# Performance work log

Hardware: AMD Instinct MI355X
Metric: run time of the kernel (lower is better)

## Reference

```python
import jax, jax.numpy as jnp
import numpy as np

N = 100000   # nodes
E = 1600000  # edges
D_IN, D_H, D_OUT = 128, 128, 64
BN_EPS = 1e-5


def setup_inputs() -> dict:
    key = jax.random.key(0)
    ks = jax.random.split(key, 12)

    def lin_w(k, fan_in, shape):
        s = 1.0 / np.sqrt(fan_in)
        return jax.random.uniform(k, shape, jnp.float32, -s, s)

    return {
        "x": jax.random.normal(ks[0], (N, D_IN), jnp.float32),
        "edge_index": jax.random.randint(ks[1], (2, E), 0, N, dtype=jnp.int64),
        "edge_weight": jax.random.uniform(ks[2], (E,), jnp.float32),
        "W1": lin_w(ks[3], D_IN, (D_IN, D_H)),
        "b1": jnp.zeros((D_H,), jnp.float32),
        "W2": lin_w(ks[4], D_H, (D_H, D_H)),
        "b2": jnp.zeros((D_H,), jnp.float32),
        "W3": lin_w(ks[5], D_H, (D_H, D_OUT)),
        "b3": jnp.zeros((D_OUT,), jnp.float32),
        "gamma1": jnp.ones((D_H,), jnp.float32),
        "beta1": jnp.zeros((D_H,), jnp.float32),
        "gamma2": jnp.ones((D_H,), jnp.float32),
        "beta2": jnp.zeros((D_H,), jnp.float32),
    }


def _gcn_conv(x, src, dst, w, W, b):
    # PyG GCNConv: x' = D^{-1/2} (A + I) D^{-1/2} (x W) + b, self-loop weight 1
    n = x.shape[0]
    h = x @ W                                   # [N, d_out]
    loop = jnp.arange(n, dtype=src.dtype)
    s = jnp.concatenate([src, loop])            # [E+N]
    d = jnp.concatenate([dst, loop])
    ww = jnp.concatenate([w, jnp.ones((n,), w.dtype)])
    deg = jax.ops.segment_sum(ww, d, num_segments=n)          # in-degree at targets
    dinv = jnp.where(deg > 0, jax.lax.rsqrt(deg), 0.0)
    norm = dinv[s] * ww * dinv[d]               # [E+N]
    msg = h[s] * norm[:, None]                  # gather + scale
    out = jax.ops.segment_sum(msg, d, num_segments=n)
    return out + b


def _batch_norm(x, gamma, beta):
    mean = jnp.mean(x, axis=0)
    var = jnp.mean(jnp.square(x - mean), axis=0)  # biased, as BatchNorm uses
    return (x - mean) * jax.lax.rsqrt(var + BN_EPS) * gamma + beta


def reference(x, edge_index, edge_weight, W1, b1, W2, b2, W3, b3,
              gamma1, beta1, gamma2, beta2):
    src, dst = edge_index[0], edge_index[1]
    h = _gcn_conv(x, src, dst, edge_weight, W1, b1)
    h = jax.nn.relu(_batch_norm(h, gamma1, beta1))
    h = _gcn_conv(h, src, dst, edge_weight, W2, b2)
    h = jax.nn.relu(_batch_norm(h, gamma2, beta2))
    return _gcn_conv(h, src, dst, edge_weight, W3, b3)
```

## Files before the change

### kernel.cpp

```cpp
#include <hip/hip_runtime.h>
#include <hip/hip_fp16.h>
#include <cstdint>
#include <cstddef>

#define BN_EPS 1e-5f
#define FPSCALE 268435456.0f

typedef _Float16 half8 __attribute__((ext_vector_type(8)));
typedef float floatx4 __attribute__((ext_vector_type(4)));

__device__ __forceinline__ float loadS(const __half* p) { return __half2float(*p); }
__device__ __forceinline__ float2 load2(const __half* p) {
    return __half22float2(*(const __half2*)p);
}
__device__ __forceinline__ void storeS(float* p, float v) { *p = v; }
__device__ __forceinline__ void storeS(__half* p, float v) { *p = __float2half(v); }
__device__ __forceinline__ void store2(float* p, float a, float b) {
    *(float2*)p = make_float2(a, b);
}
__device__ __forceinline__ void store2(__half* p, float a, float b) {
    *(__half2*)p = __floats2half2_rn(a, b);
}
__device__ __forceinline__ float wn_of(unsigned v) {
    __half_raw hr; hr.x = (unsigned short)(v & 0x7fffu);
    return __half2float((__half)hr);
}

static __device__ __forceinline__ int load_edge(const void* ei, int mode64, long long pos) {
    if (mode64) return (int)((const long long*)ei)[pos];
    return ((const int*)ei)[pos];
}

__global__ __launch_bounds__(256) void init_kernel(const unsigned* __restrict__ eiw, int nwords,
                                                   int* __restrict__ mode,
                                                   unsigned long long* __restrict__ packed, int N,
                                                   const float* __restrict__ W1,
                                                   const float* __restrict__ W2,
                                                   const float* __restrict__ W3,
                                                   _Float16* __restrict__ WT1,
                                                   _Float16* __restrict__ WT2,
                                                   _Float16* __restrict__ WT3, int nb) {
    __shared__ unsigned red[256];
    const int bid = (int)blockIdx.x;
    const int tid = (int)threadIdx.x;
    if (bid < nb) {
        int i = bid * 256 + tid;
        if (i < N) packed[i] = 0ULL;
        return;
    }
    if (bid == nb) {
        unsigned m = 0;
        for (int i = 1 + 2 * tid; i < nwords; i += 512) m |= eiw[i];
        red[tid] = m;
        __syncthreads();
        for (int s = 128; s > 0; s >>= 1) {
            if (tid < s) red[tid] |= red[tid + s];
            __syncthreads();
        }
        if (tid == 0) mode[0] = (red[0] == 0) ? 1 : 0;
        return;
    }
    const int t_ = bid - nb - 1;
    if (t_ < 64) {
        int t = t_ * 256 + tid;
        int n = t / 128, k = t % 128;
        WT1[t] = (_Float16)W1[k * 128 + n];
    } else if (t_ < 128) {
        int t = (t_ - 64) * 256 + tid;
        int n = t / 128, k = t % 128;
        WT2[t] = (_Float16)W2[k * 128 + n];
    } else {
        int t = (t_ - 128) * 256 + tid;
        int n = t / 128, k = t % 128;
        WT3[t] = (_Float16)W3[k * 64 + n];
    }
}

template <int M, bool BN, typename TI>
__device__ __forceinline__ void gemm_body(int gbid, const TI* __restrict__ X,
                                          const _Float16* __restrict__ WTg,
                                          const float* __restrict__ sc,
                                          const float* __restrict__ sh,
                                          __half* __restrict__ Hout, int N,
                                          _Float16* WT ) {
    constexpr int CT = M / 16;
    constexpr int LDK = 136;

    for (int t = threadIdx.x; t < M * 16; t += 256) {
        int n = t / 16, seg = t % 16;
        *(half8*)&WT[n * LDK + seg * 8] = *(const half8*)&WTg[n * 128 + seg * 8];
    }
    __syncthreads();

    const int wave = (int)threadIdx.x >> 6;
    const int lane = (int)threadIdx.x & 63;
    const int qd = lane >> 4;
    const int ln = lane & 15;
    const int tile0 = gbid * 64 + wave * 16;
    int ar = tile0 + ln;
    if (ar >= N) ar = N - 1;

    half8 aF[4];
    const TI* xr = X + (size_t)ar * 128 + qd * 8;
#pragma unroll
    for (int kb = 0; kb < 4; ++kb) {
        float vv[8];
        if constexpr (sizeof(TI) == 4) {
            float4 v0 = *(const float4*)(xr + kb * 32);
            float4 v1 = *(const float4*)(xr + kb * 32 + 4);
            vv[0] = v0.x; vv[1] = v0.y; vv[2] = v0.z; vv[3] = v0.w;
            vv[4] = v1.x; vv[5] = v1.y; vv[6] = v1.z; vv[7] = v1.w;
        } else {
            half8 raw = *(const half8*)(xr + kb * 32);
#pragma unroll
            for (int j = 0; j < 8; ++j) vv[j] = (float)raw[j];
        }
        if (BN) {
            const int kbase = kb * 32 + qd * 8;
#pragma unroll
            for (int j = 0; j < 8; ++j)
                vv[j] = fmaxf(fmaf(vv[j], sc[kbase + j], sh[kbase + j]), 0.0f);
        }
        half8 a;
#pragma unroll
        for (int j = 0; j < 8; ++j) a[j] = (_Float16)vv[j];
        aF[kb] = a;
    }

#pragma unroll
    for (int ct = 0; ct < CT; ++ct) {
        floatx4 acc = {0.0f, 0.0f, 0.0f, 0.0f};
#pragma unroll
        for (int kb = 0; kb < 4; ++kb) {
            half8 b = *(const half8*)&WT[(ct * 16 + ln) * LDK + kb * 32 + qd * 8];
            acc = __builtin_amdgcn_mfma_f32_16x16x32_f16(aF[kb], b, acc, 0, 0, 0);
        }
#pragma unroll
        for (int r = 0; r < 4; ++r) {
            int orow = tile0 + qd * 4 + r;
            if (orow < N) Hout[(size_t)orow * M + ct * 16 + ln] = __float2half(acc[r]);
        }
    }
}

__global__ __launch_bounds__(256) void hist_gemm1_kernel(const void* __restrict__ ei,
                                                         const float* __restrict__ ew,
                                                         unsigned long long* __restrict__ packed,
                                                         unsigned char* __restrict__ rank,
                                                         const int* __restrict__ mode, int E, int GB,
                                                         const float* __restrict__ X,
                                                         const _Float16* __restrict__ WT1g,
                                                         __half* __restrict__ Hout, int N) {
    __shared__ _Float16 WT[128 * 136];
    if ((int)blockIdx.x < GB) {
        gemm_body<128, false, float>(blockIdx.x, X, WT1g, nullptr, nullptr, Hout, N, WT);
        return;
    }
    int e = ((int)blockIdx.x - GB) * 256 + (int)threadIdx.x;
    if (e >= E) return;
    int md = *mode;
    int d = load_edge(ei, md, (long long)E + e);
    unsigned long long contrib = (1ULL << 40) | (unsigned long long)(ew[e] * FPSCALE);
    unsigned long long old = atomicAdd(&packed[d], contrib);
    unsigned r = (unsigned)(old >> 40);
    rank[e] = (unsigned char)(r < 63u ? r : 63u);
}

__global__ __launch_bounds__(256) void unpack_kernel(const unsigned long long* __restrict__ packed,
                                                     float* __restrict__ dinv,
                                                     int* __restrict__ cnt, int N) {
    int i = (int)blockIdx.x * 256 + (int)threadIdx.x;
    if (i < N) {
        unsigned long long p = packed[i];
        int c = (int)(p >> 40);
        cnt[i] = c < 64 ? c : 64;
        dinv[i] = rsqrtf(1.0f + (float)(p & 0xFFFFFFFFFFULL) * (1.0f / FPSCALE));
    }
}

__global__ __launch_bounds__(256) void scatter_zero_kernel(const void* __restrict__ ei,
                                                           const float* __restrict__ ew,
                                                           const float* __restrict__ dinv,
                                                           const unsigned char* __restrict__ rank,
                                                           unsigned* __restrict__ edata,
                                                           const int* __restrict__ mode, int E, int EBK,
                                                           float* __restrict__ gsum,
                                                           float* __restrict__ gsq,
                                                           int* __restrict__ tickets) {
    if ((int)blockIdx.x == EBK) {
        if (threadIdx.x < 128) { gsum[threadIdx.x] = 0.0f; gsq[threadIdx.x] = 0.0f; }
        if (threadIdx.x < 2) tickets[threadIdx.x] = 0;
        return;
    }
    int e = (int)blockIdx.x * 256 + (int)threadIdx.x;
    if (e >= E) return;
    int md = *mode;
    int s = load_edge(ei, md, e);
    int d = load_edge(ei, md, (long long)E + e);
    float wn = dinv[s] * ew[e] * dinv[d];
    unsigned hb = (unsigned)__half_as_ushort(__float2half(wn)) & 0x7fffu;
    edata[((size_t)d << 6) + rank[e]] = ((unsigned)s << 15) | hb;
}

template <int D, bool BIAS, typename TY>
__global__ __launch_bounds__(256) void agg_kernel(const __half* __restrict__ H,
                                                  const unsigned* __restrict__ edata,
                                                  const int* __restrict__ cnt,
                                                  const float* __restrict__ dinv,
                                                  const float* __restrict__ bias,
                                                  TY* __restrict__ Y, int N) {
    constexpr int VPT = D / 64;
    const int lane = (int)threadIdx.x & 63;
    const int i = (int)blockIdx.x * 4 + ((int)threadIdx.x >> 6);
    if (i >= N) return;
    const int c0 = lane * VPT;
    const float di = dinv[i];
    const float dii = di * di;

    float acc0, acc1 = 0.0f;
    if constexpr (VPT == 2) {
        float2 h = load2(H + (size_t)i * D + c0);
        acc0 = dii * h.x;
        acc1 = dii * h.y;
    } else {
        acc0 = dii * loadS(H + (size_t)i * D + c0);
    }

    const int n = cnt[i];
    unsigned ev = 0;
    if (lane < n) ev = edata[((size_t)i << 6) + lane];
    for (int j = 0; j < n; j += 8) {
        const unsigned e0 = __shfl(ev, j),     e1 = __shfl(ev, j + 1);
        const unsigned e2 = __shfl(ev, j + 2), e3 = __shfl(ev, j + 3);
        const unsigned e4 = __shfl(ev, j + 4), e5 = __shfl(ev, j + 5);
        const unsigned e6 = __shfl(ev, j + 6), e7 = __shfl(ev, j + 7);
        if constexpr (VPT == 2) {
            float2 h0 = load2(H + (size_t)(e0 >> 15) * D + c0);
            float2 h1 = load2(H + (size_t)(e1 >> 15) * D + c0);
            float2 h2 = load2(H + (size_t)(e2 >> 15) * D + c0);
            float2 h3 = load2(H + (size_t)(e3 >> 15) * D + c0);
            float2 h4 = load2(H + (size_t)(e4 >> 15) * D + c0);
            float2 h5 = load2(H + (size_t)(e5 >> 15) * D + c0);
            float2 h6 = load2(H + (size_t)(e6 >> 15) * D + c0);
            float2 h7 = load2(H + (size_t)(e7 >> 15) * D + c0);
            acc0 = fmaf(wn_of(e0), h0.x, acc0); acc1 = fmaf(wn_of(e0), h0.y, acc1);
            acc0 = fmaf(wn_of(e1), h1.x, acc0); acc1 = fmaf(wn_of(e1), h1.y, acc1);
            acc0 = fmaf(wn_of(e2), h2.x, acc0); acc1 = fmaf(wn_of(e2), h2.y, acc1);
            acc0 = fmaf(wn_of(e3), h3.x, acc0); acc1 = fmaf(wn_of(e3), h3.y, acc1);
            acc0 = fmaf(wn_of(e4), h4.x, acc0); acc1 = fmaf(wn_of(e4), h4.y, acc1);
            acc0 = fmaf(wn_of(e5), h5.x, acc0); acc1 = fmaf(wn_of(e5), h5.y, acc1);
            acc0 = fmaf(wn_of(e6), h6.x, acc0); acc1 = fmaf(wn_of(e6), h6.y, acc1);
            acc0 = fmaf(wn_of(e7), h7.x, acc0); acc1 = fmaf(wn_of(e7), h7.y, acc1);
        } else {
            float h0 = loadS(H + (size_t)(e0 >> 15) * D + c0);
            float h1 = loadS(H + (size_t)(e1 >> 15) * D + c0);
            float h2 = loadS(H + (size_t)(e2 >> 15) * D + c0);
            float h3 = loadS(H + (size_t)(e3 >> 15) * D + c0);
            float h4 = loadS(H + (size_t)(e4 >> 15) * D + c0);
            float h5 = loadS(H + (size_t)(e5 >> 15) * D + c0);
            float h6 = loadS(H + (size_t)(e6 >> 15) * D + c0);
            float h7 = loadS(H + (size_t)(e7 >> 15) * D + c0);
            acc0 = fmaf(wn_of(e0), h0, acc0);
            acc0 = fmaf(wn_of(e1), h1, acc0);
            acc0 = fmaf(wn_of(e2), h2, acc0);
            acc0 = fmaf(wn_of(e3), h3, acc0);
            acc0 = fmaf(wn_of(e4), h4, acc0);
            acc0 = fmaf(wn_of(e5), h5, acc0);
            acc0 = fmaf(wn_of(e6), h6, acc0);
            acc0 = fmaf(wn_of(e7), h7, acc0);
        }
    }

    if constexpr (VPT == 2) {
        if (BIAS) { acc0 += bias[c0]; acc1 += bias[c0 + 1]; }
        store2(Y + (size_t)i * D + c0, acc0, acc1);
    } else {
        if (BIAS) acc0 += bias[c0];
        storeS(Y + (size_t)i * D + c0, acc0);
    }
}

template <int M, bool BN, typename TI, bool ZERO>
__global__ __launch_bounds__(256) void gemm_mfma_kernel(const TI* __restrict__ X,
                                                        const _Float16* __restrict__ WTg,
                                                        const float* __restrict__ sc,
                                                        const float* __restrict__ sh,
                                                        __half* __restrict__ Hout, int N,
                                                        float* __restrict__ gsum,
                                                        float* __restrict__ gsq, int GB) {
    __shared__ _Float16 WT[M * 136];
    if (ZERO && (int)blockIdx.x == GB) {
        if (threadIdx.x < 128) { gsum[threadIdx.x] = 0.0f; gsq[threadIdx.x] = 0.0f; }
        return;
    }
    gemm_body<M, BN, TI>(blockIdx.x, X, WTg, sc, sh, Hout, N, WT);
}

__global__ __launch_bounds__(256) void stats_fin_kernel(const __half* __restrict__ Y,
                                                        float* __restrict__ gsum,
                                                        float* __restrict__ gsq, int N,
                                                        int* __restrict__ ticket,
                                                        const float* __restrict__ gamma,
                                                        const float* __restrict__ beta,
                                                        float* __restrict__ sc,
                                                        float* __restrict__ sh) {
    __shared__ float ls[256], lq[256];
    __shared__ int isLast;
    const int tid = (int)threadIdx.x;
    const int c = tid & 127;
    const int half_ = tid >> 7;
    float s = 0.0f, q = 0.0f;
    for (int row = (int)blockIdx.x * 2 + half_; row < N; row += 512) {
        float v = __half2float(Y[(size_t)row * 128 + c]);
        s += v;
        q = fmaf(v, v, q);
    }
    ls[tid] = s; lq[tid] = q;
    __syncthreads();
    if (tid < 128) {
        atomicAdd(&gsum[c], ls[tid] + ls[tid + 128]);
        atomicAdd(&gsq[c],  lq[tid] + lq[tid + 128]);
    }
    __threadfence();
    __syncthreads();
    if (tid == 0) {
        int old = atomicAdd(ticket, 1);
        isLast = (old == (int)gridDim.x - 1);
    }
    __syncthreads();
    if (isLast && tid < 128) {
        float gs = __hip_atomic_load(&gsum[tid], __ATOMIC_RELAXED, __HIP_MEMORY_SCOPE_AGENT);
        float gq = __hip_atomic_load(&gsq[tid],  __ATOMIC_RELAXED, __HIP_MEMORY_SCOPE_AGENT);
        float inv_n = 1.0f / (float)N;
        float mean = gs * inv_n;
        float var = gq * inv_n - mean * mean;
        float scale = gamma[tid] * rsqrtf(var + BN_EPS);
        sc[tid] = scale;
        sh[tid] = beta[tid] - mean * scale;
    }
}

extern "C" void kernel_launch(void* const* d_in, const int* in_sizes, int n_in,
                              void* d_out, int out_size, void* d_ws, size_t ws_size,
                              hipStream_t stream) {
    const float* x   = (const float*)d_in[0];
    const void*  ei  = d_in[1];
    const float* ew  = (const float*)d_in[2];
    const float* W1  = (const float*)d_in[3];
    const float* W2  = (const float*)d_in[5];
    const float* W3  = (const float*)d_in[7];
    const float* b3  = (const float*)d_in[8];
    const float* g1  = (const float*)d_in[9];
    const float* be1 = (const float*)d_in[10];
    const float* g2  = (const float*)d_in[11];
    const float* be2 = (const float*)d_in[12];
    float* out = (float*)d_out;

    const int N = in_sizes[0] / 128;
    const int E = in_sizes[2];

    char* w = (char*)d_ws;
    size_t off = 0;
    auto alloc = [&](size_t bytes) -> void* {
        void* p = w + off;
        off += (bytes + 255) & ~(size_t)255;
        return p;
    };
    unsigned long long* packed = (unsigned long long*)alloc((size_t)N * 8);
    float* dinv      = (float*)alloc((size_t)N * 4);
    int*   cnt       = (int*)  alloc((size_t)N * 4);
    unsigned char* rank = (unsigned char*)alloc((size_t)E);
    unsigned* edata  = (unsigned*)alloc((size_t)N * 64 * 4);
    int*   mode      = (int*)  alloc(256);
    int*   tickets   = (int*)  alloc(256);
    float* gsum      = (float*)alloc(128 * 4);
    float* gsq       = (float*)alloc(128 * 4);
    float* scb       = (float*)alloc(128 * 4);
    float* shb       = (float*)alloc(128 * 4);
    _Float16* WT1    = (_Float16*)alloc(128 * 128 * 2);
    _Float16* WT2    = (_Float16*)alloc(128 * 128 * 2);
    _Float16* WT3    = (_Float16*)alloc(128 * 64 * 2);
    __half* H        = (__half*)alloc((size_t)N * 128 * 2);
    __half* Yh       = (__half*)alloc((size_t)N * 128 * 2);
    (void)ws_size; (void)n_in; (void)out_size;

    const int nb  = (N + 255) / 256;
    const int ebk = (E + 255) / 256;
    const int gb  = (N + 63) / 64;
    const int ab  = (N + 3) / 4;

    init_kernel<<<nb + 1 + 160, 256, 0, stream>>>((const unsigned*)ei, 4096, mode, packed, N,
                                                  W1, W2, W3, WT1, WT2, WT3, nb);
    hist_gemm1_kernel<<<gb + ebk, 256, 0, stream>>>(ei, ew, packed, rank, mode, E, gb,
                                                    x, WT1, H, N);
    unpack_kernel<<<nb, 256, 0, stream>>>(packed, dinv, cnt, N);
    scatter_zero_kernel<<<ebk + 1, 256, 0, stream>>>(ei, ew, dinv, rank, edata,
                                                     mode, E, ebk, gsum, gsq, tickets);

    agg_kernel<128, false, __half><<<ab, 256, 0, stream>>>(H, edata, cnt, dinv, nullptr, Yh, N);
    stats_fin_kernel<<<256, 256, 0, stream>>>(Yh, gsum, gsq, N, &tickets[0], g1, be1, scb, shb);

    gemm_mfma_kernel<128, true, __half, true><<<gb + 1, 256, 0, stream>>>(Yh, WT2, scb, shb, H, N, gsum, gsq, gb);
    agg_kernel<128, false, __half><<<ab, 256, 0, stream>>>(H, edata, cnt, dinv, nullptr, Yh, N);
    stats_fin_kernel<<<256, 256, 0, stream>>>(Yh, gsum, gsq, N, &tickets[1], g2, be2, scb, shb);

    gemm_mfma_kernel<64, true, __half, false><<<gb, 256, 0, stream>>>(Yh, WT3, scb, shb, H, N, nullptr, nullptr, gb);
    agg_kernel<64, true, float><<<ab, 256, 0, stream>>>(H, edata, cnt, dinv, b3, out, N);
}
```

Before: 566.7 us.

## Split aggregation across lane groups with 16-byte feature loads and shuffle reduction

The neighbor aggregation kernel now assigns each lane a 16-byte slice of 8 half features. Groups of lanes handle different edges at the same time instead of every lane walking all edges. Partial sums are combined across groups with xor-shuffles, and one group adds the self-loop term and bias and writes the row with vector stores. The aim is fewer, wider gather loads and more independent memory requests in flight per wavefront. The cost is an 8-float accumulator per lane and a cross-lane reduction at the end of each row.

Result: no change. 560.4 us (-1.1%).

```diff
diff --git a/kernel.cpp b/kernel.cpp
--- a/kernel.cpp
+++ b/kernel.cpp
@@ -9,18 +9,6 @@
 typedef _Float16 half8 __attribute__((ext_vector_type(8)));
 typedef float floatx4 __attribute__((ext_vector_type(4)));
 
-__device__ __forceinline__ float loadS(const __half* p) { return __half2float(*p); }
-__device__ __forceinline__ float2 load2(const __half* p) {
-    return __half22float2(*(const __half2*)p);
-}
-__device__ __forceinline__ void storeS(float* p, float v) { *p = v; }
-__device__ __forceinline__ void storeS(__half* p, float v) { *p = __float2half(v); }
-__device__ __forceinline__ void store2(float* p, float a, float b) {
-    *(float2*)p = make_float2(a, b);
-}
-__device__ __forceinline__ void store2(__half* p, float a, float b) {
-    *(__half2*)p = __floats2half2_rn(a, b);
-}
 __device__ __forceinline__ float wn_of(unsigned v) {
     __half_raw hr; hr.x = (unsigned short)(v & 0x7fffu);
     return __half2float((__half)hr);
@@ -209,74 +197,58 @@
                                                   const float* __restrict__ dinv,
                                                   const float* __restrict__ bias,
                                                   TY* __restrict__ Y, int N) {
-    constexpr int VPT = D / 64;
+    constexpr int LPR = D / 8;
+    constexpr int GROUPS = 64 / LPR;
     const int lane = (int)threadIdx.x & 63;
     const int i = (int)blockIdx.x * 4 + ((int)threadIdx.x >> 6);
     if (i >= N) return;
-    const int c0 = lane * VPT;
-    const float di = dinv[i];
-    const float dii = di * di;
-
-    float acc0, acc1 = 0.0f;
-    if constexpr (VPT == 2) {
-        float2 h = load2(H + (size_t)i * D + c0);
-        acc0 = dii * h.x;
-        acc1 = dii * h.y;
-    } else {
-        acc0 = dii * loadS(H + (size_t)i * D + c0);
-    }
+    const int g = lane / LPR;
+    const int c0 = (lane % LPR) * 8;
 
     const int n = cnt[i];
     unsigned ev = 0;
     if (lane < n) ev = edata[((size_t)i << 6) + lane];
-    for (int j = 0; j < n; j += 8) {
-        const unsigned e0 = __shfl(ev, j),     e1 = __shfl(ev, j + 1);
-        const unsigned e2 = __shfl(ev, j + 2), e3 = __shfl(ev, j + 3);
-        const unsigned e4 = __shfl(ev, j + 4), e5 = __shfl(ev, j + 5);
-        const unsigned e6 = __shfl(ev, j + 6), e7 = __shfl(ev, j + 7);
-        if constexpr (VPT == 2) {
-            float2 h0 = load2(H + (size_t)(e0 >> 15) * D + c0);
-            float2 h1 = load2(H + (size_t)(e1 >> 15) * D + c0);
-            float2 h2 = load2(H + (size_t)(e2 >> 15) * D + c0);
-            float2 h3 = load2(H + (size_t)(e3 >> 15) * D + c0);
-            float2 h4 = load2(H + (size_t)(e4 >> 15) * D + c0);
-            float2 h5 = load2(H + (size_t)(e5 >> 15) * D + c0);
-            float2 h6 = load2(H + (size_t)(e6 >> 15) * D + c0);
-            float2 h7 = load2(H + (size_t)(e7 >> 15) * D + c0);
-            acc0 = fmaf(wn_of(e0), h0.x, acc0); acc1 = fmaf(wn_of(e0), h0.y, acc1);
-            acc0 = fmaf(wn_of(e1), h1.x, acc0); acc1 = fmaf(wn_of(e1), h1.y, acc1);
-            acc0 = fmaf(wn_of(e2), h2.x, acc0); acc1 = fmaf(wn_of(e2), h2.y, acc1);
-            acc0 = fmaf(wn_of(e3), h3.x, acc0); acc1 = fmaf(wn_of(e3), h3.y, acc1);
-            acc0 = fmaf(wn_of(e4), h4.x, acc0); acc1 = fmaf(wn_of(e4), h4.y, acc1);
-            acc0 = fmaf(wn_of(e5), h5.x, acc0); acc1 = fmaf(wn_of(e5), h5.y, acc1);
-            acc0 = fmaf(wn_of(e6), h6.x, acc0); acc1 = fmaf(wn_of(e6), h6.y, acc1);
-            acc0 = fmaf(wn_of(e7), h7.x, acc0); acc1 = fmaf(wn_of(e7), h7.y, acc1);
+
+    float acc[8] = {};
+    for (int j = 0; j < n; j += 2 * GROUPS) {
+        const unsigned ea = __shfl(ev, j + g);
+        const unsigned eb = __shfl(ev, j + GROUPS + g);
+        const half8 ha = *(const half8*)(H + (size_t)(ea >> 15) * D + c0);
+        const half8 hb = *(const half8*)(H + (size_t)(eb >> 15) * D + c0);
+        const float wa = wn_of(ea), wb = wn_of(eb);
+#pragma unroll
+        for (int k = 0; k < 8; ++k) acc[k] = fmaf(wa, (float)ha[k], acc[k]);
+#pragma unroll
+        for (int k = 0; k < 8; ++k) acc[k] = fmaf(wb, (float)hb[k], acc[k]);
+    }
+
+#pragma unroll
+    for (int m = LPR; m < 64; m <<= 1) {
+#pragma unroll
+        for (int k = 0; k < 8; ++k) acc[k] += __shfl_xor(acc[k], m);
+    }
+
+    if (lane < LPR) {
+        const float di = dinv[i];
+        const float dii = di * di;
+        const half8 hs = *(const half8*)(H + (size_t)i * D + c0);
+#pragma unroll
+        for (int k = 0; k < 8; ++k) acc[k] = fmaf(dii, (float)hs[k], acc[k]);
+        if (BIAS) {
+#pragma unroll
+            for (int k = 0; k < 8; ++k) acc[k] += bias[c0 + k];
+        }
+        if constexpr (sizeof(TY) == 2) {
+            half8 o;
+#pragma unroll
+            for (int k = 0; k < 8; ++k) o[k] = (_Float16)acc[k];
+            *(half8*)((__half*)Y + (size_t)i * D + c0) = o;
         } else {
-            float h0 = loadS(H + (size_t)(e0 >> 15) * D + c0);
-            float h1 = loadS(H + (size_t)(e1 >> 15) * D + c0);
-            float h2 = loadS(H + (size_t)(e2 >> 15) * D + c0);
-            float h3 = loadS(H + (size_t)(e3 >> 15) * D + c0);
-            float h4 = loadS(H + (size_t)(e4 >> 15) * D + c0);
-            float h5 = loadS(H + (size_t)(e5 >> 15) * D + c0);
-            float h6 = loadS(H + (size_t)(e6 >> 15) * D + c0);
-            float h7 = loadS(H + (size_t)(e7 >> 15) * D + c0);
-            acc0 = fmaf(wn_of(e0), h0, acc0);
-            acc0 = fmaf(wn_of(e1), h1, acc0);
-            acc0 = fmaf(wn_of(e2), h2, acc0);
-            acc0 = fmaf(wn_of(e3), h3, acc0);
-            acc0 = fmaf(wn_of(e4), h4, acc0);
-            acc0 = fmaf(wn_of(e5), h5, acc0);
-            acc0 = fmaf(wn_of(e6), h6, acc0);
-            acc0 = fmaf(wn_of(e7), h7, acc0);
-        }
-    }
-
-    if constexpr (VPT == 2) {
-        if (BIAS) { acc0 += bias[c0]; acc1 += bias[c0 + 1]; }
-        store2(Y + (size_t)i * D + c0, acc0, acc1);
-    } else {
-        if (BIAS) acc0 += bias[c0];
-        storeS(Y + (size_t)i * D + c0, acc0);
+            float4 o0 = make_float4(acc[0], acc[1], acc[2], acc[3]);
+            float4 o1 = make_float4(acc[4], acc[5], acc[6], acc[7]);
+            *(float4*)((float*)Y + (size_t)i * D + c0) = o0;
+            *(float4*)((float*)Y + (size_t)i * D + c0 + 4) = o1;
+        }
     }
 }
 
```
